# Kernel optimization log

Hardware: AMD Instinct MI355X
Metric: run time of the kernel (lower is better)

The kernel has to match this reference:

```python
import jax, jax.numpy as jnp
import numpy as np

UINT8_MAX = 255.0
SUBPIXEL_EPS = 1e-6
MAX_SUBPIXEL_MAGNITUDE = 1.0


def spiral_pattern_np(sz):
    """Spiral traversal pattern, identical to the torch reference."""
    pattern = np.zeros((2 * sz + 1, 2 * sz + 1), dtype=np.float32)
    radius = sz
    n = 0
    for dy in range(radius + 1):
        for direction in range(4):
            limit = 1 if (direction == 0 and dy == 0) else dy
            for dx in range(-dy, limit):
                if direction == 0:
                    wx, wy = radius + dx, radius + dy
                elif direction == 1:
                    wx, wy = radius + dy, radius - dx
                elif direction == 2:
                    wx, wy = radius - dx, radius - dy
                else:
                    wx, wy = radius - dy, radius + dx
                n += 1
                pattern[wy, wx] = n
    return pattern


def binomial(img):
    # separable [1 2 1]/4 blur, replicate padding; img: [B,1,H,W]
    p = jnp.pad(img, ((0, 0), (0, 0), (1, 1), (0, 0)), mode='edge')
    v = (p[:, :, :-2, :] + 2.0 * img + p[:, :, 2:, :]) / 4.0
    p = jnp.pad(v, ((0, 0), (0, 0), (0, 0), (1, 1)), mode='edge')
    return (p[:, :, :, :-2] + 2.0 * v + p[:, :, :, 2:]) / 4.0


def gradient(f):
    p = jnp.pad(f, ((0, 0), (0, 0), (1, 1), (1, 1)), mode='edge')
    gy = (p[:, :, 2:, 1:-1] - p[:, :, :-2, 1:-1]) / 2.0
    gx = (p[:, :, 1:-1, 2:] - p[:, :, 1:-1, :-2]) / 2.0
    return gy, gx


def blocks(img, T):
    # [B,1,H,W] -> non-overlapping T x T templates flattened: [B, H//T, W//T, T*T]
    B = img.shape[0]
    H, W = img.shape[2], img.shape[3]
    x = img.reshape(B, H // T, T, W // T, T)
    return x.transpose(0, 1, 3, 2, 4).reshape(B, H // T, W // T, T * T)


def calculate_flow(img_cur, img_prev, T, R):
    cur = binomial(img_cur)
    prev = binomial(img_prev)
    # emulate cast-to-uint8 quantization of the reference pipeline
    q = lambda x: jnp.clip(jnp.round(x * UINT8_MAX), 0.0, UINT8_MAX)
    cur_q, prev_q = q(cur), q(prev)

    templates = blocks(cur_q, T)                       # [B,Hb,Wb,T2]
    B, Hb, Wb, T2 = templates.shape
    H, W = img_cur.shape[2], img_cur.shape[3]

    # candidate shifted blocks (search windows): [B,Hb,Wb,C,T2], C=(2R+1)^2
    pad_prev = jnp.pad(prev_q, ((0, 0), (0, 0), (R, R), (R, R)), mode='edge')
    cands = [blocks(pad_prev[:, :, R + dy:R + dy + H, R + dx:R + dx + W], T)
             for dy in range(-R, R + 1) for dx in range(-R, R + 1)]
    windows = jnp.stack(cands, axis=3)

    # SAD cost volume: [B,Hb,Wb,C]
    cost = jnp.sum(jnp.abs(windows - templates[:, :, :, None, :]), axis=-1)

    # spiral-tie-break argmin (equivalent to ArgMinCentered mode='spiral':
    # among min-cost candidates, pick the one earliest in the spiral order)
    spir = jnp.asarray(spiral_pattern_np(R).reshape(-1), dtype=jnp.float32)
    min_c = jnp.min(cost, axis=-1, keepdims=True)
    tie = jnp.where(cost == min_c, spir, jnp.inf)
    idx = jnp.argmin(tie, axis=-1)                     # [B,Hb,Wb]

    rng = jnp.arange(-R, R + 1, dtype=jnp.float32)
    jj, ii = jnp.meshgrid(rng, rng, indexing='ij')
    vec_lut = -1.0 * jnp.stack([jj, ii], axis=-1).reshape(-1, 2)
    vec = vec_lut[idx]                                 # [B,Hb,Wb,2] = [-dy,-dx]

    # 3x3 median filter (replicate pad) on the vector field [B,2,Hb,Wb]
    v = vec.transpose(0, 3, 1, 2)
    vp = jnp.pad(v, ((0, 0), (0, 0), (1, 1), (1, 1)), mode='edge')
    patches = jnp.stack([vp[:, :, i:i + Hb, j:j + Wb]
                         for i in range(3) for j in range(3)], axis=2)
    v_med = jnp.median(patches, axis=2)                # [B,2,Hb,Wb]

    # gather the matched block at the (rounded) median vector
    med_i = jnp.clip(jnp.round(v_med), -R, R).astype(jnp.int32)
    off_y, off_x = -med_i[:, 0], -med_i[:, 1]          # vec stores negated offsets
    cand_idx = (off_y + R) * (2 * R + 1) + (off_x + R) # [B,Hb,Wb]
    idxe = jnp.broadcast_to(cand_idx[..., None, None], (B, Hb, Wb, 1, T2))
    matched = jnp.take_along_axis(windows, idxe, axis=3)[:, :, :, 0, :]

    # Lucas-Kanade subpixel refinement (border-ring weighted)
    tmpl = templates / UINT8_MAX
    mat = matched / UINT8_MAX
    gy_img, gx_img = gradient(cur)
    gy = blocks(gy_img, T)
    gx = blocks(gx_img, T)
    pred = jnp.pad(jnp.zeros((T - 2, T - 2), jnp.float32), ((1, 1), (1, 1)),
                   constant_values=1.0).reshape(-1)
    rs = lambda x: jnp.sum(x, axis=-1)                 # [B,Hb,Wb]
    a = rs(gx * gx * pred)
    b = rs(gx * gy * pred)
    d = rs(gy * gy * pred)
    diff = mat - tmpl
    p = rs(diff * gx * pred)
    qv = rs(diff * gy * pred)
    det = a * d - b * b
    safe_det = jnp.where(det <= SUBPIXEL_EPS, 1.0, det)
    sub_u = (d * p - b * qv) / safe_det
    sub_v = (a * qv - b * p) / safe_det
    sub = jnp.stack([sub_v, sub_u], axis=-1)           # [B,Hb,Wb,2] (y,x)
    invalid = (det[..., None] <= SUBPIXEL_EPS) | (jnp.abs(sub) >= MAX_SUBPIXEL_MAGNITUDE)
    sub = jnp.where(invalid, 0.0, sub)

    flow = v_med + sub.transpose(0, 3, 1, 2)           # [B,2,Hb,Wb]
    return flow.astype(jnp.float32)


def setup_inputs() -> dict:
    key = jax.random.key(0)
    k1, k2 = jax.random.split(key)
    img_cur = jax.random.uniform(k1, (1, 1, 544, 960), dtype=jnp.float32)
    img_prev = jax.random.uniform(k2, (1, 1, 544, 960), dtype=jnp.float32)
    return {"img_cur": img_cur, "img_prev": img_prev,
            "template_sz": 8, "search_range": 4}


def reference(img_cur, img_prev, template_sz, search_range):
    return calculate_flow(img_cur, img_prev, template_sz, search_range)
```

## Files before the change

kernel.cpp:

```cpp
#include <hip/hip_runtime.h>

#define H  544
#define W  960
#define T  8
#define R  4
#define HB (H / T)
#define WB (W / T)
#define NB (HB * WB)
#define NC 81
#define WIN 16

__device__ __forceinline__ int iclamp(int v, int lo, int hi) {
    return v < lo ? lo : (v > hi ? hi : v);
}

struct SpiralTab { int v[NC]; };

__host__ __device__ constexpr SpiralTab make_spiral() {
    SpiralTab t{};
    int n = 0;
    for (int dy = 0; dy <= R; ++dy) {
        for (int dir = 0; dir < 4; ++dir) {
            int limit = (dir == 0 && dy == 0) ? 1 : dy;
            for (int dx = -dy; dx < limit; ++dx) {
                int wx, wy;
                if (dir == 0)      { wx = R + dx; wy = R + dy; }
                else if (dir == 1) { wx = R + dy; wy = R - dx; }
                else if (dir == 2) { wx = R - dx; wy = R - dy; }
                else               { wx = R - dy; wy = R + dx; }
                t.v[n] = (wy << 4) | wx;
                ++n;
            }
        }
    }
    return t;
}

static __constant__ SpiralTab SPIR = make_spiral();

__device__ __forceinline__ unsigned int sadu8(unsigned int a, unsigned int b, unsigned int acc) {
#if __has_builtin(__builtin_amdgcn_sad_u8)
    return __builtin_amdgcn_sad_u8(a, b, acc);
#else
    unsigned int d;
    asm("v_sad_u8 %0, %1, %2, %3" : "=v"(d) : "v"(a), "v"(b), "v"(acc));
    return d;
#endif
}

__device__ __forceinline__ unsigned int alignb(unsigned int hi, unsigned int lo, unsigned int sh) {
#if __has_builtin(__builtin_amdgcn_alignbyte)
    return __builtin_amdgcn_alignbyte(hi, lo, sh);
#else
    unsigned int d;
    asm("v_alignbyte_b32 %0, %1, %2, %3" : "=v"(d) : "v"(hi), "v"(lo), "v"(sh));
    return d;
#endif
}

__global__ void __launch_bounds__(256)
k_blur(const float* __restrict__ cur, const float* __restrict__ prev,
       float* __restrict__ cur_blur,
       unsigned char* __restrict__ cur_q,
       unsigned char* __restrict__ prev_q) {
    int img = blockIdx.y;
    int p   = blockIdx.x * 256 + threadIdx.x;
    int y  = p / 240;
    int xq = p % 240;
    int x0 = xq * 4;
    const float* src = (img == 0) ? cur : prev;
    int ym = iclamp(y - 1, 0, H - 1) * W;
    int y0 = y * W;
    int yp = iclamp(y + 1, 0, H - 1) * W;
    int xl = (x0 == 0) ? 0 : x0 - 1;
    int xr = (x0 + 4 > W - 1) ? W - 1 : x0 + 4;

    float4 rm = *(const float4*)(src + ym + x0);
    float4 rc = *(const float4*)(src + y0 + x0);
    float4 rp = *(const float4*)(src + yp + x0);
    float lm = src[ym + xl], lc = src[y0 + xl], lp = src[yp + xl];
    float em = src[ym + xr], ec = src[y0 + xr], ep = src[yp + xr];

#define VERT(a, b, c) (__fmul_rn(__fadd_rn(__fadd_rn((a), __fmul_rn(2.0f, (b))), (c)), 0.25f))
    float vL = VERT(lm, lc, lp);
    float v0 = VERT(rm.x, rc.x, rp.x);
    float v1 = VERT(rm.y, rc.y, rp.y);
    float v2 = VERT(rm.z, rc.z, rp.z);
    float v3 = VERT(rm.w, rc.w, rp.w);
    float vR = VERT(em, ec, ep);
    float h0 = VERT(vL, v0, v1);
    float h1 = VERT(v0, v1, v2);
    float h2 = VERT(v1, v2, v3);
    float h3 = VERT(v2, v3, vR);
#undef VERT
#define QU(h) ((unsigned int)fminf(fmaxf(rintf(__fmul_rn((h), 255.0f)), 0.0f), 255.0f))
    unsigned int packed = QU(h0) | (QU(h1) << 8) | (QU(h2) << 16) | (QU(h3) << 24);
#undef QU
    if (img == 0) {
        *(float4*)(cur_blur + y0 + x0) = make_float4(h0, h1, h2, h3);
        *(unsigned int*)(cur_q + y0 + x0) = packed;
    } else {
        *(unsigned int*)(prev_q + y0 + x0) = packed;
    }
}

__global__ void __launch_bounds__(256)
k_sad(const unsigned char* __restrict__ cur_q,
      const unsigned char* __restrict__ prev_q,
      float* __restrict__ vecy, float* __restrict__ vecx) {
    __shared__ uint4 region[4][WIN];
    __shared__ uint2 tmplS[4][T];
    int w    = threadIdx.x >> 6;
    int lane = threadIdx.x & 63;
    int bidx = blockIdx.x * 4 + w;
    int byi = bidx / WB, bxi = bidx % WB;
    int by0 = byi * T, bx0 = bxi * T;

    {
        int ry = lane >> 2, wx = lane & 3;
        int gy = iclamp(by0 - R + ry, 0, H - 1);
        unsigned int word;
        if (bxi > 0 && bxi < WB - 1) {
            word = *(const unsigned int*)(prev_q + gy * W + (bx0 - 4 + wx * 4));
        } else {
            int xb = bx0 - 4 + wx * 4;
            unsigned int b0 = prev_q[gy * W + iclamp(xb + 0, 0, W - 1)];
            unsigned int b1 = prev_q[gy * W + iclamp(xb + 1, 0, W - 1)];
            unsigned int b2 = prev_q[gy * W + iclamp(xb + 2, 0, W - 1)];
            unsigned int b3 = prev_q[gy * W + iclamp(xb + 3, 0, W - 1)];
            word = b0 | (b1 << 8) | (b2 << 16) | (b3 << 24);
        }
        ((unsigned int*)&region[w][0])[lane] = word;
    }
    if (lane < 16) {
        int ty = lane >> 1, half = lane & 1;
        ((unsigned int*)&tmplS[w][0])[lane] =
            *(const unsigned int*)(cur_q + (by0 + ty) * W + bx0 + half * 4);
    }
    __syncthreads();

    unsigned int t0[T], t1[T];
#pragma unroll
    for (int ty = 0; ty < T; ++ty) {
        uint2 tt = tmplS[w][ty];
        t0[ty] = tt.x;
        t1[ty] = tt.y;
    }

    int cell0 = SPIR.v[lane];
    int dy0 = cell0 >> 4, dx0 = cell0 & 15;
    bool v1 = (lane + 64) < NC;
    int cell1 = SPIR.v[v1 ? (lane + 64) : 0];
    int dy1 = cell1 >> 4, dx1 = cell1 & 15;

    unsigned int sad0 = 0, sad1 = 0;
    int q0 = dx0 >> 2; unsigned int r0 = (unsigned int)(dx0 & 3);
    int q1 = dx1 >> 2; unsigned int r1 = (unsigned int)(dx1 & 3);
#pragma unroll
    for (int ty = 0; ty < T; ++ty) {
        {
            uint4 row = region[w][ty + dy0];
            unsigned int w0 = (q0 == 0) ? row.x : ((q0 == 1) ? row.y : row.z);
            unsigned int w1 = (q0 == 0) ? row.y : ((q0 == 1) ? row.z : row.w);
            unsigned int w2 = (q0 == 0) ? row.z : row.w;
            sad0 = sadu8(alignb(w1, w0, r0), t0[ty], sad0);
            sad0 = sadu8(alignb(w2, w1, r0), t1[ty], sad0);
        }
        if (v1) {
            uint4 row = region[w][ty + dy1];
            unsigned int w0 = (q1 == 0) ? row.x : ((q1 == 1) ? row.y : row.z);
            unsigned int w1 = (q1 == 0) ? row.y : ((q1 == 1) ? row.z : row.w);
            unsigned int w2 = (q1 == 0) ? row.z : row.w;
            sad1 = sadu8(alignb(w1, w0, r1), t0[ty], sad1);
            sad1 = sadu8(alignb(w2, w1, r1), t1[ty], sad1);
        }
    }

    int key = (int)((sad0 << 7) | (unsigned int)lane);
    if (v1) {
        int k1 = (int)((sad1 << 7) | (unsigned int)(lane + 64));
        key = min(key, k1);
    }
#pragma unroll
    for (int off = 32; off > 0; off >>= 1)
        key = min(key, __shfl_xor(key, off));
    if (lane == 0) {
        int rank = key & 127;
        int cell = SPIR.v[rank];
        int dyi = (cell >> 4) - R;
        int dxi = (cell & 15) - R;
        vecy[bidx] = (float)(-dyi);
        vecx[bidx] = (float)(-dxi);
    }
}

__device__ __forceinline__ void msort(float& a, float& b) {
    float mn = fminf(a, b), mx = fmaxf(a, b);
    a = mn; b = mx;
}

__device__ __forceinline__ float median9(float p[9]) {
    msort(p[1], p[2]); msort(p[4], p[5]); msort(p[7], p[8]);
    msort(p[0], p[1]); msort(p[3], p[4]); msort(p[6], p[7]);
    msort(p[1], p[2]); msort(p[4], p[5]); msort(p[7], p[8]);
    msort(p[0], p[3]); msort(p[5], p[8]); msort(p[4], p[7]);
    msort(p[3], p[6]); msort(p[1], p[4]); msort(p[2], p[5]);
    msort(p[4], p[7]); msort(p[4], p[2]); msort(p[6], p[4]);
    msort(p[4], p[2]);
    return p[4];
}

__global__ void __launch_bounds__(256)
k_flow(const unsigned char* __restrict__ cur_q,
       const unsigned char* __restrict__ prev_q,
       const float* __restrict__ cur_blur,
       const float* __restrict__ vecy, const float* __restrict__ vecx,
       float* __restrict__ out) {
    int bidx = blockIdx.x * 8 + (threadIdx.x >> 5);
    int lane = threadIdx.x & 31;
    int byi = bidx / WB, bxi = bidx % WB;

    float py[9], px[9];
#pragma unroll
    for (int i = 0; i < 3; ++i)
#pragma unroll
        for (int j = 0; j < 3; ++j) {
            int yy = iclamp(byi + i - 1, 0, HB - 1);
            int xx = iclamp(bxi + j - 1, 0, WB - 1);
            py[i * 3 + j] = vecy[yy * WB + xx];
            px[i * 3 + j] = vecx[yy * WB + xx];
        }
    float vmy = median9(py);
    float vmx = median9(px);

    int med_y = iclamp((int)rintf(vmy), -R, R);
    int med_x = iclamp((int)rintf(vmx), -R, R);
    int off_y = -med_y, off_x = -med_x;

    bool act = lane < 28;
    int k = act ? lane : 0;
    int ty, tx;
    if (k < 8)       { ty = 0;      tx = k;      }
    else if (k < 16) { ty = T - 1;  tx = k - 8;  }
    else if (k < 22) { ty = k - 15; tx = 0;      }
    else             { ty = k - 21; tx = T - 1;  }

    int by0 = byi * T, bx0 = bxi * T;
    int y = by0 + ty, x = bx0 + tx;
    float tmplv = (float)cur_q[y * W + x] / 255.0f;
    int my = iclamp(y + off_y, 0, H - 1);
    int mx = iclamp(x + off_x, 0, W - 1);
    float matv = (float)prev_q[my * W + mx] / 255.0f;
    float gyv = (cur_blur[iclamp(y + 1, 0, H - 1) * W + x]
               - cur_blur[iclamp(y - 1, 0, H - 1) * W + x]) * 0.5f;
    float gxv = (cur_blur[y * W + iclamp(x + 1, 0, W - 1)]
               - cur_blur[y * W + iclamp(x - 1, 0, W - 1)]) * 0.5f;
    float diff = matv - tmplv;

    float a = act ? gxv * gxv : 0.0f;
    float b = act ? gxv * gyv : 0.0f;
    float d = act ? gyv * gyv : 0.0f;
    float p = act ? diff * gxv : 0.0f;
    float q = act ? diff * gyv : 0.0f;
#pragma unroll
    for (int off = 16; off > 0; off >>= 1) {
        a += __shfl_xor(a, off);
        b += __shfl_xor(b, off);
        d += __shfl_xor(d, off);
        p += __shfl_xor(p, off);
        q += __shfl_xor(q, off);
    }

    if (lane == 0) {
        float det  = a * d - b * b;
        float safe = (det <= 1e-6f) ? 1.0f : det;
        float su = (d * p - b * q) / safe;
        float sv = (a * q - b * p) / safe;
        bool inval = (det <= 1e-6f);
        float sy = (inval || fabsf(sv) >= 1.0f) ? 0.0f : sv;
        float sx = (inval || fabsf(su) >= 1.0f) ? 0.0f : su;
        out[bidx]      = vmy + sy;
        out[NB + bidx] = vmx + sx;
    }
}

extern "C" void kernel_launch(void* const* d_in, const int* in_sizes, int n_in,
                              void* d_out, int out_size, void* d_ws, size_t ws_size,
                              hipStream_t stream) {
    const float* cur  = (const float*)d_in[0];
    const float* prev = (const float*)d_in[1];
    float* out = (float*)d_out;

    char* ws = (char*)d_ws;
    float*         cur_blur = (float*)ws;
    unsigned char* cur_q    = (unsigned char*)(ws + (size_t)H * W * 4);
    unsigned char* prev_q   = cur_q + (size_t)H * W;
    float*         vecy     = (float*)(ws + (size_t)H * W * 6);
    float*         vecx     = vecy + NB;

    k_blur<<<dim3(H * 240 / 256, 2), 256, 0, stream>>>(cur, prev, cur_blur, cur_q, prev_q);
    k_sad<<<NB / 4, 256, 0, stream>>>(cur_q, prev_q, vecy, vecx);
    k_flow<<<NB / 8, 256, 0, stream>>>(cur_q, prev_q, cur_blur, vecy, vecx, out);
}
```

Measured before the change: 75.47 us.

## Fuse blur and quantization into SAD kernel with per-block halo recompute

Removes the separate blur kernel and computes the binomial blur plus uint8 quantization inside the SAD kernel. Each wave computes the vertical pass for its 16x18 search window of prev and its 8x10 template region of cur into shared memory, then finishes the horizontal pass directly into the byte region and template. The block interior is still written to prev_q, cur_q and cur_blur for the later flow kernel. This saves one launch and the global round trip of the quantized images, at the cost of redundant halo blur work and scalar, uncoalesced float loads.

```diff
diff --git a/kernel.cpp b/kernel.cpp
--- a/kernel.cpp
+++ b/kernel.cpp
@@ -58,84 +58,66 @@
 #endif
 }
 
+#define VERT(a, b, c) (__fmul_rn(__fadd_rn(__fadd_rn((a), __fmul_rn(2.0f, (b))), (c)), 0.25f))
+#define QU(h) ((unsigned int)fminf(fmaxf(rintf(__fmul_rn((h), 255.0f)), 0.0f), 255.0f))
+
 __global__ void __launch_bounds__(256)
-k_blur(const float* __restrict__ cur, const float* __restrict__ prev,
-       float* __restrict__ cur_blur,
-       unsigned char* __restrict__ cur_q,
-       unsigned char* __restrict__ prev_q) {
-    int img = blockIdx.y;
-    int p   = blockIdx.x * 256 + threadIdx.x;
-    int y  = p / 240;
-    int xq = p % 240;
-    int x0 = xq * 4;
-    const float* src = (img == 0) ? cur : prev;
-    int ym = iclamp(y - 1, 0, H - 1) * W;
-    int y0 = y * W;
-    int yp = iclamp(y + 1, 0, H - 1) * W;
-    int xl = (x0 == 0) ? 0 : x0 - 1;
-    int xr = (x0 + 4 > W - 1) ? W - 1 : x0 + 4;
-
-    float4 rm = *(const float4*)(src + ym + x0);
-    float4 rc = *(const float4*)(src + y0 + x0);
-    float4 rp = *(const float4*)(src + yp + x0);
-    float lm = src[ym + xl], lc = src[y0 + xl], lp = src[yp + xl];
-    float em = src[ym + xr], ec = src[y0 + xr], ep = src[yp + xr];
-
-#define VERT(a, b, c) (__fmul_rn(__fadd_rn(__fadd_rn((a), __fmul_rn(2.0f, (b))), (c)), 0.25f))
-    float vL = VERT(lm, lc, lp);
-    float v0 = VERT(rm.x, rc.x, rp.x);
-    float v1 = VERT(rm.y, rc.y, rp.y);
-    float v2 = VERT(rm.z, rc.z, rp.z);
-    float v3 = VERT(rm.w, rc.w, rp.w);
-    float vR = VERT(em, ec, ep);
-    float h0 = VERT(vL, v0, v1);
-    float h1 = VERT(v0, v1, v2);
-    float h2 = VERT(v1, v2, v3);
-    float h3 = VERT(v2, v3, vR);
-#undef VERT
-#define QU(h) ((unsigned int)fminf(fmaxf(rintf(__fmul_rn((h), 255.0f)), 0.0f), 255.0f))
-    unsigned int packed = QU(h0) | (QU(h1) << 8) | (QU(h2) << 16) | (QU(h3) << 24);
-#undef QU
-    if (img == 0) {
-        *(float4*)(cur_blur + y0 + x0) = make_float4(h0, h1, h2, h3);
-        *(unsigned int*)(cur_q + y0 + x0) = packed;
-    } else {
-        *(unsigned int*)(prev_q + y0 + x0) = packed;
-    }
-}
-
-__global__ void __launch_bounds__(256)
-k_sad(const unsigned char* __restrict__ cur_q,
-      const unsigned char* __restrict__ prev_q,
-      float* __restrict__ vecy, float* __restrict__ vecx) {
+k_blur_sad(const float* __restrict__ cur, const float* __restrict__ prev,
+           float* __restrict__ cur_blur,
+           unsigned char* __restrict__ cur_q,
+           unsigned char* __restrict__ prev_q,
+           float* __restrict__ vecy, float* __restrict__ vecx) {
+    __shared__ float vb[4][WIN][20];
+    __shared__ float vc[4][T][12];
     __shared__ uint4 region[4][WIN];
     __shared__ uint2 tmplS[4][T];
+
     int w    = threadIdx.x >> 6;
     int lane = threadIdx.x & 63;
     int bidx = blockIdx.x * 4 + w;
     int byi = bidx / WB, bxi = bidx % WB;
     int by0 = byi * T, bx0 = bxi * T;
 
+    for (int e = lane; e < WIN * 18; e += 64) {
+        int ry = e / 18, cx = e - ry * 18;
+        int gy = iclamp(by0 - R + ry, 0, H - 1);
+        int gx = iclamp(bx0 - 5 + cx, 0, W - 1);
+        int ym = iclamp(gy - 1, 0, H - 1) * W;
+        int yp = iclamp(gy + 1, 0, H - 1) * W;
+        vb[w][ry][cx] = VERT(prev[ym + gx], prev[gy * W + gx], prev[yp + gx]);
+    }
+    for (int e = lane; e < T * 10; e += 64) {
+        int ty = e / 10, cx = e - ty * 10;
+        int gy = by0 + ty;
+        int gx = iclamp(bx0 - 1 + cx, 0, W - 1);
+        int ym = iclamp(gy - 1, 0, H - 1) * W;
+        int yp = iclamp(gy + 1, 0, H - 1) * W;
+        vc[w][ty][cx] = VERT(cur[ym + gx], cur[gy * W + gx], cur[yp + gx]);
+    }
+    __syncthreads();
+
     {
-        int ry = lane >> 2, wx = lane & 3;
-        int gy = iclamp(by0 - R + ry, 0, H - 1);
-        unsigned int word;
-        if (bxi > 0 && bxi < WB - 1) {
-            word = *(const unsigned int*)(prev_q + gy * W + (bx0 - 4 + wx * 4));
-        } else {
-            int xb = bx0 - 4 + wx * 4;
-            unsigned int b0 = prev_q[gy * W + iclamp(xb + 0, 0, W - 1)];
-            unsigned int b1 = prev_q[gy * W + iclamp(xb + 1, 0, W - 1)];
-            unsigned int b2 = prev_q[gy * W + iclamp(xb + 2, 0, W - 1)];
-            unsigned int b3 = prev_q[gy * W + iclamp(xb + 3, 0, W - 1)];
-            word = b0 | (b1 << 8) | (b2 << 16) | (b3 << 24);
-        }
-        ((unsigned int*)&region[w][0])[lane] = word;
-    }
-    if (lane < 16) {
-        int ty = lane >> 1, half = lane & 1;
-        ((unsigned int*)&tmplS[w][0])[lane] =
-            *(const unsigned int*)(cur_q + (by0 + ty) * W + bx0 + half * 4);
+        unsigned char* regB = (unsigned char*)&region[w][0];
+        int base = bx0 - 5;
+        for (int e = lane; e < WIN * WIN; e += 64) {
+            int ry = e >> 4, rx = e & 15;
+            int gxp = iclamp(bx0 - R + rx, 0, W - 1);
+            int xm = (gxp > 0) ? gxp - 1 : 0;
+            int xp = (gxp < W - 1) ? gxp + 1 : W - 1;
+            float h = VERT(vb[w][ry][xm - base], vb[w][ry][gxp - base], vb[w][ry][xp - base]);
+            unsigned char b = (unsigned char)QU(h);
+            regB[ry * 16 + rx] = b;
+            if (ry >= R && ry < R + T && rx >= R && rx < R + T)
+                prev_q[(by0 + ry - R) * W + (bx0 + rx - R)] = b;
+        }
+    }
+    {
+        int ty = lane >> 3, tx = lane & 7;
+        float h = VERT(vc[w][ty][tx], vc[w][ty][tx + 1], vc[w][ty][tx + 2]);
+        unsigned char b = (unsigned char)QU(h);
+        ((unsigned char*)&tmplS[w][0])[ty * 8 + tx] = b;
+        cur_q[(by0 + ty) * W + bx0 + tx] = b;
+        cur_blur[(by0 + ty) * W + bx0 + tx] = h;
     }
     __syncthreads();
 
@@ -298,7 +280,6 @@
     float*         vecy     = (float*)(ws + (size_t)H * W * 6);
     float*         vecx     = vecy + NB;
 
-    k_blur<<<dim3(H * 240 / 256, 2), 256, 0, stream>>>(cur, prev, cur_blur, cur_q, prev_q);
-    k_sad<<<NB / 4, 256, 0, stream>>>(cur_q, prev_q, vecy, vecx);
+    k_blur_sad<<<NB / 4, 256, 0, stream>>>(cur, prev, cur_blur, cur_q, prev_q, vecy, vecx);
     k_flow<<<NB / 8, 256, 0, stream>>>(cur_q, prev_q, cur_blur, vecy, vecx, out);
 }
```

After: 76.50 us. About the same (+1.4%).

## Fuse SAD search and flow refinement into one kernel with tagged spin-wait

Applied to the files above, without the earlier changes.

Merges the block-matching SAD kernel and the median/subpixel flow kernel into one launch. Each wave publishes its integer vector as a tagged 32-bit word. Neighbouring waves spin on those words with relaxed agent-scope atomics before taking the 3x3 median. The refinement step now reads template and matched pixels from the shared-memory tiles already loaded for the SAD search, instead of reloading them from global memory. The cost removed is one kernel launch plus the round trip of the vectors through global memory. The risks are deadlock if not all blocks are co-resident, and stale tags left in the workspace from a previous call, which could let a wave read old vectors.

```diff
diff --git a/kernel.cpp b/kernel.cpp
--- a/kernel.cpp
+++ b/kernel.cpp
@@ -9,6 +9,7 @@
 #define NB (HB * WB)
 #define NC 81
 #define WIN 16
+#define TAG 0x51C0u
 
 __device__ __forceinline__ int iclamp(int v, int lo, int hi) {
     return v < lo ? lo : (v > hi ? hi : v);
@@ -104,17 +105,44 @@
     }
 }
 
-__global__ void __launch_bounds__(256)
-k_sad(const unsigned char* __restrict__ cur_q,
-      const unsigned char* __restrict__ prev_q,
-      float* __restrict__ vecy, float* __restrict__ vecx) {
+__device__ __forceinline__ void msort(float& a, float& b) {
+    float mn = fminf(a, b), mx = fmaxf(a, b);
+    a = mn; b = mx;
+}
+
+__device__ __forceinline__ float median9(float p[9]) {
+    msort(p[1], p[2]); msort(p[4], p[5]); msort(p[7], p[8]);
+    msort(p[0], p[1]); msort(p[3], p[4]); msort(p[6], p[7]);
+    msort(p[1], p[2]); msort(p[4], p[5]); msort(p[7], p[8]);
+    msort(p[0], p[3]); msort(p[5], p[8]); msort(p[4], p[7]);
+    msort(p[3], p[6]); msort(p[1], p[4]); msort(p[2], p[5]);
+    msort(p[4], p[7]); msort(p[4], p[2]); msort(p[6], p[4]);
+    msort(p[4], p[2]);
+    return p[4];
+}
+
+__device__ __forceinline__ unsigned int wait_word(unsigned int* p) {
+    unsigned int v = __hip_atomic_load(p, __ATOMIC_RELAXED, __HIP_MEMORY_SCOPE_AGENT);
+    while ((v >> 16) != TAG) {
+        __builtin_amdgcn_s_sleep(1);
+        v = __hip_atomic_load(p, __ATOMIC_RELAXED, __HIP_MEMORY_SCOPE_AGENT);
+    }
+    return v;
+}
+
+__global__ void __launch_bounds__(256, 8)
+k_sadflow(const unsigned char* __restrict__ cur_q,
+          const unsigned char* __restrict__ prev_q,
+          const float* __restrict__ cur_blur,
+          unsigned int* __restrict__ vecw,
+          float* __restrict__ out) {
     __shared__ uint4 region[4][WIN];
     __shared__ uint2 tmplS[4][T];
-    int w    = threadIdx.x >> 6;
-    int lane = threadIdx.x & 63;
-    int bidx = blockIdx.x * 4 + w;
-    int byi = bidx / WB, bxi = bidx % WB;
-    int by0 = byi * T, bx0 = bxi * T;
+    const int wv   = (int)(threadIdx.x >> 6);
+    const int lane = (int)(threadIdx.x & 63);
+    const int bidx = (int)blockIdx.x * 4 + wv;
+    const int byi = bidx / WB, bxi = bidx % WB;
+    const int by0 = byi * T, bx0 = bxi * T;
 
     {
         int ry = lane >> 2, wx = lane & 3;
@@ -130,22 +158,14 @@
             unsigned int b3 = prev_q[gy * W + iclamp(xb + 3, 0, W - 1)];
             word = b0 | (b1 << 8) | (b2 << 16) | (b3 << 24);
         }
-        ((unsigned int*)&region[w][0])[lane] = word;
+        ((unsigned int*)&region[wv][0])[lane] = word;
     }
     if (lane < 16) {
         int ty = lane >> 1, half = lane & 1;
-        ((unsigned int*)&tmplS[w][0])[lane] =
+        ((unsigned int*)&tmplS[wv][0])[lane] =
             *(const unsigned int*)(cur_q + (by0 + ty) * W + bx0 + half * 4);
     }
     __syncthreads();
-
-    unsigned int t0[T], t1[T];
-#pragma unroll
-    for (int ty = 0; ty < T; ++ty) {
-        uint2 tt = tmplS[w][ty];
-        t0[ty] = tt.x;
-        t1[ty] = tt.y;
-    }
 
     int cell0 = SPIR.v[lane];
     int dy0 = cell0 >> 4, dx0 = cell0 & 15;
@@ -158,24 +178,24 @@
     int q1 = dx1 >> 2; unsigned int r1 = (unsigned int)(dx1 & 3);
 #pragma unroll
     for (int ty = 0; ty < T; ++ty) {
+        uint2 tt = tmplS[wv][ty];
         {
-            uint4 row = region[w][ty + dy0];
+            uint4 row = region[wv][ty + dy0];
             unsigned int w0 = (q0 == 0) ? row.x : ((q0 == 1) ? row.y : row.z);
             unsigned int w1 = (q0 == 0) ? row.y : ((q0 == 1) ? row.z : row.w);
             unsigned int w2 = (q0 == 0) ? row.z : row.w;
-            sad0 = sadu8(alignb(w1, w0, r0), t0[ty], sad0);
-            sad0 = sadu8(alignb(w2, w1, r0), t1[ty], sad0);
+            sad0 = sadu8(alignb(w1, w0, r0), tt.x, sad0);
+            sad0 = sadu8(alignb(w2, w1, r0), tt.y, sad0);
         }
         if (v1) {
-            uint4 row = region[w][ty + dy1];
+            uint4 row = region[wv][ty + dy1];
             unsigned int w0 = (q1 == 0) ? row.x : ((q1 == 1) ? row.y : row.z);
             unsigned int w1 = (q1 == 0) ? row.y : ((q1 == 1) ? row.z : row.w);
             unsigned int w2 = (q1 == 0) ? row.z : row.w;
-            sad1 = sadu8(alignb(w1, w0, r1), t0[ty], sad1);
-            sad1 = sadu8(alignb(w2, w1, r1), t1[ty], sad1);
-        }
-    }
-
+            sad1 = sadu8(alignb(w1, w0, r1), tt.x, sad1);
+            sad1 = sadu8(alignb(w2, w1, r1), tt.y, sad1);
+        }
+    }
     int key = (int)((sad0 << 7) | (unsigned int)lane);
     if (v1) {
         int k1 = (int)((sad1 << 7) | (unsigned int)(lane + 64));
@@ -187,48 +207,21 @@
     if (lane == 0) {
         int rank = key & 127;
         int cell = SPIR.v[rank];
-        int dyi = (cell >> 4) - R;
-        int dxi = (cell & 15) - R;
-        vecy[bidx] = (float)(-dyi);
-        vecx[bidx] = (float)(-dxi);
-    }
-}
-
-__device__ __forceinline__ void msort(float& a, float& b) {
-    float mn = fminf(a, b), mx = fmaxf(a, b);
-    a = mn; b = mx;
-}
-
-__device__ __forceinline__ float median9(float p[9]) {
-    msort(p[1], p[2]); msort(p[4], p[5]); msort(p[7], p[8]);
-    msort(p[0], p[1]); msort(p[3], p[4]); msort(p[6], p[7]);
-    msort(p[1], p[2]); msort(p[4], p[5]); msort(p[7], p[8]);
-    msort(p[0], p[3]); msort(p[5], p[8]); msort(p[4], p[7]);
-    msort(p[3], p[6]); msort(p[1], p[4]); msort(p[2], p[5]);
-    msort(p[4], p[7]); msort(p[4], p[2]); msort(p[6], p[4]);
-    msort(p[4], p[2]);
-    return p[4];
-}
-
-__global__ void __launch_bounds__(256)
-k_flow(const unsigned char* __restrict__ cur_q,
-       const unsigned char* __restrict__ prev_q,
-       const float* __restrict__ cur_blur,
-       const float* __restrict__ vecy, const float* __restrict__ vecx,
-       float* __restrict__ out) {
-    int bidx = blockIdx.x * 8 + (threadIdx.x >> 5);
-    int lane = threadIdx.x & 31;
-    int byi = bidx / WB, bxi = bidx % WB;
+        int vy = -((cell >> 4) - R);
+        int vx = -((cell & 15) - R);
+        unsigned int word = (TAG << 16) | ((unsigned int)(vy + 8) << 8) | (unsigned int)(vx + 8);
+        __hip_atomic_store(&vecw[bidx], word, __ATOMIC_RELAXED, __HIP_MEMORY_SCOPE_AGENT);
+    }
 
     float py[9], px[9];
 #pragma unroll
     for (int i = 0; i < 3; ++i)
 #pragma unroll
         for (int j = 0; j < 3; ++j) {
-            int yy = iclamp(byi + i - 1, 0, HB - 1);
-            int xx = iclamp(bxi + j - 1, 0, WB - 1);
-            py[i * 3 + j] = vecy[yy * WB + xx];
-            px[i * 3 + j] = vecx[yy * WB + xx];
+            int nb = iclamp(byi + i - 1, 0, HB - 1) * WB + iclamp(bxi + j - 1, 0, WB - 1);
+            unsigned int wd = wait_word(&vecw[nb]);
+            py[i * 3 + j] = (float)((int)((wd >> 8) & 255u) - 8);
+            px[i * 3 + j] = (float)((int)(wd & 255u) - 8);
         }
     float vmy = median9(py);
     float vmx = median9(px);
@@ -239,29 +232,36 @@
 
     bool act = lane < 28;
     int k = act ? lane : 0;
-    int ty, tx;
-    if (k < 8)       { ty = 0;      tx = k;      }
-    else if (k < 16) { ty = T - 1;  tx = k - 8;  }
-    else if (k < 22) { ty = k - 15; tx = 0;      }
-    else             { ty = k - 21; tx = T - 1;  }
-
-    int by0 = byi * T, bx0 = bxi * T;
-    int y = by0 + ty, x = bx0 + tx;
-    float tmplv = (float)cur_q[y * W + x] / 255.0f;
-    int my = iclamp(y + off_y, 0, H - 1);
-    int mx = iclamp(x + off_x, 0, W - 1);
-    float matv = (float)prev_q[my * W + mx] / 255.0f;
-    float gyv = (cur_blur[iclamp(y + 1, 0, H - 1) * W + x]
-               - cur_blur[iclamp(y - 1, 0, H - 1) * W + x]) * 0.5f;
-    float gxv = (cur_blur[y * W + iclamp(x + 1, 0, W - 1)]
-               - cur_blur[y * W + iclamp(x - 1, 0, W - 1)]) * 0.5f;
-    float diff = matv - tmplv;
-
-    float a = act ? gxv * gxv : 0.0f;
-    float b = act ? gxv * gyv : 0.0f;
-    float d = act ? gyv * gyv : 0.0f;
-    float p = act ? diff * gxv : 0.0f;
-    float q = act ? diff * gyv : 0.0f;
+    int rty, rtx;
+    if (k < 8)       { rty = 0;      rtx = k;      }
+    else if (k < 16) { rty = T - 1;  rtx = k - 8;  }
+    else if (k < 22) { rty = k - 15; rtx = 0;      }
+    else             { rty = k - 21; rtx = T - 1;  }
+
+    float a = 0.f, b = 0.f, d = 0.f, p = 0.f, q = 0.f;
+    if (act) {
+        int y = by0 + rty, x = bx0 + rtx;
+        unsigned int tb = ((const unsigned char*)&tmplS[wv][0])[rty * 8 + rtx];
+        float tmplv = (float)tb / 255.0f;
+        int ridx = rty + off_y + 4;
+        int cidx = rtx + off_x + 4;
+        uint4 row = region[wv][ridx];
+        unsigned int wsel = (cidx >> 2) == 0 ? row.x
+                          : ((cidx >> 2) == 1 ? row.y
+                          : ((cidx >> 2) == 2 ? row.z : row.w));
+        unsigned int mb = (wsel >> ((cidx & 3) * 8)) & 255u;
+        float matv = (float)mb / 255.0f;
+        float gyv = (cur_blur[iclamp(y + 1, 0, H - 1) * W + x]
+                   - cur_blur[iclamp(y - 1, 0, H - 1) * W + x]) * 0.5f;
+        float gxv = (cur_blur[y * W + iclamp(x + 1, 0, W - 1)]
+                   - cur_blur[y * W + iclamp(x - 1, 0, W - 1)]) * 0.5f;
+        float diff = matv - tmplv;
+        a = gxv * gxv;
+        b = gxv * gyv;
+        d = gyv * gyv;
+        p = diff * gxv;
+        q = diff * gyv;
+    }
 #pragma unroll
     for (int off = 16; off > 0; off >>= 1) {
         a += __shfl_xor(a, off);
@@ -270,7 +270,6 @@
         p += __shfl_xor(p, off);
         q += __shfl_xor(q, off);
     }
-
     if (lane == 0) {
         float det  = a * d - b * b;
         float safe = (det <= 1e-6f) ? 1.0f : det;
@@ -295,10 +294,8 @@
     float*         cur_blur = (float*)ws;
     unsigned char* cur_q    = (unsigned char*)(ws + (size_t)H * W * 4);
     unsigned char* prev_q   = cur_q + (size_t)H * W;
-    float*         vecy     = (float*)(ws + (size_t)H * W * 6);
-    float*         vecx     = vecy + NB;
+    unsigned int*  vecw     = (unsigned int*)(ws + (size_t)H * W * 6);
 
     k_blur<<<dim3(H * 240 / 256, 2), 256, 0, stream>>>(cur, prev, cur_blur, cur_q, prev_q);
-    k_sad<<<NB / 4, 256, 0, stream>>>(cur_q, prev_q, vecy, vecx);
-    k_flow<<<NB / 8, 256, 0, stream>>>(cur_q, prev_q, cur_blur, vecy, vecx, out);
-}
+    k_sadflow<<<NB / 4, 256, 0, stream>>>(cur_q, prev_q, cur_blur, vecw, out);
+}
```

New measurement: 84.06 us. +11.4%, slower.
